# Performance work log

Measured on AMD Instinct MI355X. Metric: run time of the kernel, lower is better.

Reference implementation:

```python
import jax, jax.numpy as jnp
import numpy as np

HIDDEN = 2048
N_HEADS = 16
N_KV_HEADS = 4
HEAD_DIM = HIDDEN // N_HEADS  # 128
BATCH = 1
SEQ = 2048
EPS = 1e-6


def _rms_norm(x, scale, eps=EPS):
    var = jnp.mean(jnp.square(x), axis=-1, keepdims=True)
    return x * jax.lax.rsqrt(var + eps) * scale


def _rotate_half(x):
    x1, x2 = jnp.split(x, 2, axis=-1)
    return jnp.concatenate((-x2, x1), axis=-1)


def setup_inputs() -> dict:
    key = jax.random.key(0)
    ks = jax.random.split(key, 8)
    hidden_states = jax.random.normal(ks[0], (BATCH, SEQ, HIDDEN), dtype=jnp.float32)
    # causal mask, broadcastable over [B, H, S, S]
    attention_mask = jnp.tril(jnp.ones((SEQ, SEQ), dtype=bool))[None, None, :, :]
    # standard RoPE tables, broadcastable against [B, S, H, D]
    inv_freq = 1.0 / (10000.0 ** (np.arange(0, HEAD_DIM, 2, dtype=np.float32) / HEAD_DIM))
    t = np.arange(SEQ, dtype=np.float32)
    freqs = np.outer(t, inv_freq)                      # [S, D/2]
    emb = np.concatenate([freqs, freqs], axis=-1)      # [S, D]
    cos = jnp.asarray(np.cos(emb))[:, None, :]         # [S, 1, D]
    sin = jnp.asarray(np.sin(emb))[:, None, :]
    s = 1.0 / np.sqrt(HIDDEN)
    Wq = jax.random.normal(ks[1], (HIDDEN, N_HEADS * HEAD_DIM), dtype=jnp.float32) * s
    Wk = jax.random.normal(ks[2], (HIDDEN, N_KV_HEADS * HEAD_DIM), dtype=jnp.float32) * s
    Wv = jax.random.normal(ks[3], (HIDDEN, N_KV_HEADS * HEAD_DIM), dtype=jnp.float32) * s
    Wo = jax.random.normal(ks[4], (HIDDEN, HIDDEN), dtype=jnp.float32) * s
    q_norm_scale = jnp.ones((HEAD_DIM,), dtype=jnp.float32)
    k_norm_scale = jnp.ones((HEAD_DIM,), dtype=jnp.float32)
    last_norm_scale = jnp.ones((HIDDEN,), dtype=jnp.float32)
    return {
        "hidden_states": hidden_states,
        "cos": cos,
        "sin": sin,
        "Wq": Wq,
        "Wk": Wk,
        "Wv": Wv,
        "Wo": Wo,
        "q_norm_scale": q_norm_scale,
        "k_norm_scale": k_norm_scale,
        "last_norm_scale": last_norm_scale,
        "attention_mask": attention_mask,
    }


def reference(hidden_states, cos, sin, Wq, Wk, Wv, Wo,
              q_norm_scale, k_norm_scale, last_norm_scale, attention_mask):
    B, S, _ = hidden_states.shape
    q = (hidden_states @ Wq).reshape(B, S, N_HEADS, HEAD_DIM)
    k = (hidden_states @ Wk).reshape(B, S, N_KV_HEADS, HEAD_DIM)
    v = (hidden_states @ Wv).reshape(B, S, N_KV_HEADS, HEAD_DIM)
    # per-head RMSNorm on Q/K
    q = _rms_norm(q, q_norm_scale)
    k = _rms_norm(k, k_norm_scale)
    # RoPE (cos/sin broadcast [S,1,D] -> [B,S,H,D])
    q = q * cos + _rotate_half(q) * sin
    k = k * cos + _rotate_half(k) * sin
    # GQA expansion
    groups = N_HEADS // N_KV_HEADS
    if groups > 1:
        k = jnp.repeat(k, groups, axis=2)
        v = jnp.repeat(v, groups, axis=2)
    out = jax.nn.dot_product_attention(q, k, v, mask=attention_mask)  # [B,S,H,D]
    out = out.reshape(B, S, HIDDEN) @ Wo
    return _rms_norm(out, last_norm_scale)
```

## Files before the change

### kernel.cpp

```cpp
#include <hip/hip_runtime.h>

typedef unsigned short u16;
typedef unsigned int u32;

#define S 2048
#define HID 2048
#define NH 16
#define NKV 4
#define D 128
#define QKVP 3072
#define QSCALE (0.08838834764831845f * 1.4426950408889634f)
#define NEG_INF -3.0e38f

typedef __attribute__((ext_vector_type(8))) short short8;
typedef __attribute__((ext_vector_type(4))) float f32x4;

__device__ __forceinline__ float bf2f(u16 u) {
  union { u32 i; float f; } c; c.i = ((u32)u) << 16; return c.f;
}
__device__ __forceinline__ u16 f2bf(float f) {
  union { float f; u32 i; } c; c.f = f;
  u32 x = c.i;
  u32 r = x + 0x7fffu + ((x >> 16) & 1u);
  return (u16)(r >> 16);
}

#if __has_builtin(__builtin_amdgcn_exp2f)
__device__ __forceinline__ float exp2_hw(float x) { return __builtin_amdgcn_exp2f(x); }
#else
__device__ __forceinline__ float exp2_hw(float x) { return exp2f(x); }
#endif

__device__ __forceinline__ u32 cvt_pk_bf16(float a, float b) {
  u32 r;
  asm("v_cvt_pk_bf16_f32 %0, %1, %2" : "=v"(r) : "v"(a), "v"(b));
  return r;
}

__device__ __forceinline__ void gload16(const u16* g, u16* l) {
  __builtin_amdgcn_global_load_lds(
      (const __attribute__((address_space(1))) u32*)g,
      (__attribute__((address_space(3))) u32*)l, 16, 0, 0);
}

__global__ __launch_bounds__(256) void k_cvt(const float* __restrict__ src,
                                             u16* __restrict__ dst) {
  int i = (blockIdx.x * 256 + threadIdx.x) * 8;
  float4 v0 = *(const float4*)(src + i);
  float4 v1 = *(const float4*)(src + i + 4);
  ushort4 w0, w1;
  w0.x = f2bf(v0.x); w0.y = f2bf(v0.y); w0.z = f2bf(v0.z); w0.w = f2bf(v0.w);
  w1.x = f2bf(v1.x); w1.y = f2bf(v1.y); w1.z = f2bf(v1.z); w1.w = f2bf(v1.w);
  *(ushort4*)(dst + i) = w0;
  *(ushort4*)(dst + i + 4) = w1;
}

__device__ __forceinline__ void transpose_body(const float* __restrict__ src,
                                               u16* __restrict__ dst,
                                               int N, int K, int nt, int kt,
                                               int t) {
  __shared__ float T[64][65];
#pragma unroll
  for (int it = 0; it < 4; ++it) {
    int r = it * 16 + (t >> 4), c = (t & 15) * 4;
    float4 v = *(const float4*)(src + (size_t)(kt + r) * N + nt + c);
    T[r][c] = v.x; T[r][c + 1] = v.y; T[r][c + 2] = v.z; T[r][c + 3] = v.w;
  }
  __syncthreads();
#pragma unroll
  for (int it = 0; it < 2; ++it) {
    int n = it * 32 + (t >> 3), k8 = (t & 7) * 8;
    ushort4 w0, w1;
    w0.x = f2bf(T[k8 + 0][n]); w0.y = f2bf(T[k8 + 1][n]);
    w0.z = f2bf(T[k8 + 2][n]); w0.w = f2bf(T[k8 + 3][n]);
    w1.x = f2bf(T[k8 + 4][n]); w1.y = f2bf(T[k8 + 5][n]);
    w1.z = f2bf(T[k8 + 6][n]); w1.w = f2bf(T[k8 + 7][n]);
    *(ushort4*)(dst + (size_t)(nt + n) * K + kt + k8) = w0;
    *(ushort4*)(dst + (size_t)(nt + n) * K + kt + k8 + 4) = w1;
  }
}

__global__ __launch_bounds__(256) void k_transpose(const float* __restrict__ src,
                                                   u16* __restrict__ dst,
                                                   int N, int K) {
  transpose_body(src, dst, N, K, blockIdx.x * 64, blockIdx.y * 64, threadIdx.x);
}

__global__ __launch_bounds__(256) void k_transpose_qkv(const float* __restrict__ Wq,
                                                       const float* __restrict__ Wk,
                                                       const float* __restrict__ Wv,
                                                       u16* __restrict__ WT) {
  const int bx = blockIdx.x;
  const float* src; u16* dst; int N, nt;
  if (bx < 32)      { src = Wq; dst = WT;                    N = 2048; nt = bx * 64; }
  else if (bx < 40) { src = Wk; dst = WT + 2048ull * 2048;   N = 512;  nt = (bx - 32) * 64; }
  else              { src = Wv; dst = WT + 2560ull * 2048;   N = 512;  nt = (bx - 40) * 64; }
  transpose_body(src, dst, N, 2048, nt, blockIdx.y * 64, threadIdx.x);
}

__global__ __launch_bounds__(256) void k_vt(const u16* __restrict__ QKV,
                                            u16* __restrict__ Vt) {
  __shared__ u16 T[64][66];
  const int t = threadIdx.x;
  const int s0 = blockIdx.x * 64, d0 = blockIdx.y * 64;
#pragma unroll
  for (int it = 0; it < 4; ++it) {
    int r = it * 16 + (t >> 4), c = (t & 15) * 4;
    ushort4 v = *(const ushort4*)(QKV + (size_t)(s0 + r) * QKVP + 2560 + d0 + c);
    T[r][c] = v.x; T[r][c + 1] = v.y; T[r][c + 2] = v.z; T[r][c + 3] = v.w;
  }
  __syncthreads();
#pragma unroll
  for (int it = 0; it < 4; ++it) {
    int dd = it * 16 + (t >> 4), sc = (t & 15) * 4;
    ushort4 w;
    w.x = T[sc + 0][dd]; w.y = T[sc + 1][dd];
    w.z = T[sc + 2][dd]; w.w = T[sc + 3][dd];
    *(ushort4*)(Vt + (size_t)(d0 + dd) * S + s0 + sc) = w;
  }
}

__global__ __launch_bounds__(256) void k_gemm_mfma(const u16* __restrict__ A,
                                                   const u16* __restrict__ BT,
                                                   void* __restrict__ Cout,
                                                   int N, int K, int out_bf16) {
  __shared__ __align__(16) u16 As[2][128 * 32];
  __shared__ __align__(16) u16 Bs[2][128 * 32];
  const int t = threadIdx.x, w = t >> 6, lane = t & 63;
  const int l15 = lane & 15, quad = lane >> 4;
  const int m0 = blockIdx.y * 128, n0 = blockIdx.x * 128;
  const int wr = w >> 1, wc = w & 1;

  const int sr = w * 16 + (lane >> 2);
  const int sk8 = (lane & 3) * 8;
  const u16* Ag0 = A + (size_t)(m0 + sr) * K + sk8;
  const u16* Ag1 = A + (size_t)(m0 + 64 + sr) * K + sk8;
  const u16* Bg0 = BT + (size_t)(n0 + sr) * K + sk8;
  const u16* Bg1 = BT + (size_t)(n0 + 64 + sr) * K + sk8;

  f32x4 acc[4][4];
#pragma unroll
  for (int i = 0; i < 4; ++i)
#pragma unroll
    for (int j = 0; j < 4; ++j) acc[i][j] = (f32x4){0.f, 0.f, 0.f, 0.f};

  auto STAGE = [&](int k0, int b) {
    gload16(Ag0 + k0, &As[b][w * 512]);
    gload16(Ag1 + k0, &As[b][2048 + w * 512]);
    gload16(Bg0 + k0, &Bs[b][w * 512]);
    gload16(Bg1 + k0, &Bs[b][2048 + w * 512]);
  };

  STAGE(0, 0);
  __syncthreads();
  int cur = 0;
  for (int k0 = 0; k0 < K; k0 += 32) {
    if (k0 + 32 < K) STAGE(k0 + 32, cur ^ 1);

    short8 af[4], bf[4];
#pragma unroll
    for (int i = 0; i < 4; ++i)
      af[i] = *(const short8*)&As[cur][(wr * 64 + i * 16 + l15) * 32 + quad * 8];
#pragma unroll
    for (int j = 0; j < 4; ++j)
      bf[j] = *(const short8*)&Bs[cur][(wc * 64 + j * 16 + l15) * 32 + quad * 8];
#pragma unroll
    for (int i = 0; i < 4; ++i)
#pragma unroll
      for (int j = 0; j < 4; ++j)
        acc[i][j] = __builtin_amdgcn_mfma_f32_16x16x32_bf16(af[i], bf[j], acc[i][j], 0, 0, 0);

    __syncthreads();
    cur ^= 1;
  }

  if (out_bf16) {
    u16* C = (u16*)Cout;
#pragma unroll
    for (int i = 0; i < 4; ++i)
#pragma unroll
      for (int j = 0; j < 4; ++j) {
        int col = n0 + wc * 64 + j * 16 + l15;
#pragma unroll
        for (int r = 0; r < 4; ++r)
          C[(size_t)(m0 + wr * 64 + i * 16 + quad * 4 + r) * N + col] = f2bf(acc[i][j][r]);
      }
  } else {
    float* C = (float*)Cout;
#pragma unroll
    for (int i = 0; i < 4; ++i)
#pragma unroll
      for (int j = 0; j < 4; ++j) {
        int col = n0 + wc * 64 + j * 16 + l15;
#pragma unroll
        for (int r = 0; r < 4; ++r)
          C[(size_t)(m0 + wr * 64 + i * 16 + quad * 4 + r) * N + col] = acc[i][j][r];
      }
  }
}

__global__ __launch_bounds__(128) void k_norm_rope(u16* __restrict__ QKV,
                                                   const float* __restrict__ qsc,
                                                   const float* __restrict__ ksc,
                                                   const float* __restrict__ cosp,
                                                   const float* __restrict__ sinp) {
  const int s = blockIdx.x, hh = blockIdx.y, d = threadIdx.x;
  u16* row; const float* sc; float scale;
  if (hh < NH) { row = QKV + (size_t)s * QKVP + hh * D;            sc = qsc; scale = QSCALE; }
  else         { row = QKV + (size_t)s * QKVP + 2048 + (hh - NH) * D; sc = ksc; scale = 1.0f; }
  float x = bf2f(row[d]);
  float v = x * x;
#pragma unroll
  for (int o = 32; o; o >>= 1) v += __shfl_xor(v, o, 64);
  __shared__ float red[2];
  if ((d & 63) == 0) red[d >> 6] = v;
  __syncthreads();
  float var = (red[0] + red[1]) * (1.0f / 128.0f);
  float rinv = rsqrtf(var + 1e-6f) * scale;
  float xn = x * rinv * sc[d];
  __shared__ float sh[D];
  sh[d] = xn;
  __syncthreads();
  float rot = (d < 64) ? -sh[d + 64] : sh[d - 64];
  row[d] = f2bf(xn * cosp[s * D + d] + rot * sinp[s * D + d]);
}

#define KP 128
#define PTP 72

__global__ __launch_bounds__(256) void k_flash(const u16* __restrict__ QKV,
                                               const u16* __restrict__ Vt,
                                               u16* __restrict__ O) {
  const int h = blockIdx.y, g = h >> 2;
  const int qt = (h < 8) ? (31 - (int)blockIdx.x) : (int)blockIdx.x;
  const int t = threadIdx.x;
  const int w = t >> 6, lane = t & 63, l15 = lane & 15, quad = lane >> 4;

  __shared__ __align__(16) u16 Klds[2][64 * KP];
  __shared__ __align__(16) u16 Pt[4][16 * PTP];

  const int qbase = qt * 64 + w * 16;
  const int qrow = qbase + l15;

  short8 qf[4];
  {
    const u16* qp = QKV + (size_t)qrow * QKVP + h * D + quad * 8;
#pragma unroll
    for (int c = 0; c < 4; ++c) qf[c] = *(const short8*)(qp + c * 32);
  }

  float m = NEG_INF, l = 0.f;
  f32x4 oacc[8];
#pragma unroll
  for (int nc = 0; nc < 8; ++nc) oacc[nc] = (f32x4){0.f, 0.f, 0.f, 0.f};

  const int nt = qt + 1;

  auto KLOAD = [&](int j0, int b) {
#pragma unroll
    for (int it = 0; it < 4; ++it) {
      int rl = w * 16 + it * 4 + quad;
      int gchunk = (lane & 15) ^ (rl & 7);
      const u16* gp = QKV + (size_t)(j0 + rl) * QKVP + 2048 + g * D + gchunk * 8;
      gload16(gp, &Klds[b][(w * 16 + it * 4) * KP]);
    }
  };

  KLOAD(0, 0);
  for (int jt = 0; jt < nt; ++jt) {
    const int b = jt & 1;
    __syncthreads();
    if (jt + 1 < nt) KLOAD((jt + 1) * 64, b ^ 1);

    const int j0 = jt * 64;
    const u16* vbase = Vt + (size_t)g * D * S + j0;

    short8 vf0[8];
#pragma unroll
    for (int nc = 0; nc < 8; ++nc)
      vf0[nc] = *(const short8*)(vbase + (size_t)(nc * 16 + l15) * S + quad * 8);

    f32x4 sa[4];
#pragma unroll
    for (int sub = 0; sub < 4; ++sub) {
      f32x4 acc = {0.f, 0.f, 0.f, 0.f};
#pragma unroll
      for (int c = 0; c < 4; ++c) {
        int ch = (c * 4 + quad) ^ (l15 & 7);
        short8 kf = *(const short8*)&Klds[b][(sub * 16 + l15) * KP + ch * 8];
        acc = __builtin_amdgcn_mfma_f32_16x16x32_bf16(kf, qf[c], acc, 0, 0, 0);
      }
      sa[sub] = acc;
    }

    short8 vf1[8];
#pragma unroll
    for (int nc = 0; nc < 8; ++nc)
      vf1[nc] = *(const short8*)(vbase + (size_t)(nc * 16 + l15) * S + 32 + quad * 8);

    if (jt == nt - 1) {
#pragma unroll
      for (int sub = 0; sub < 4; ++sub) {
        int keyb = j0 + sub * 16 + quad * 4;
#pragma unroll
        for (int r = 0; r < 4; ++r)
          if (keyb + r > qrow) sa[sub][r] = NEG_INF;
      }
    }

    float tmax = sa[0][0];
#pragma unroll
    for (int sub = 0; sub < 4; ++sub)
#pragma unroll
      for (int r = 0; r < 4; ++r) tmax = fmaxf(tmax, sa[sub][r]);
    tmax = fmaxf(tmax, __shfl_xor(tmax, 16, 64));
    tmax = fmaxf(tmax, __shfl_xor(tmax, 32, 64));
    if (jt == 0 || !__all(tmax - m <= 8.f)) {
      float mn = (jt == 0) ? tmax : fmaxf(m, tmax);
      float alpha = (jt == 0) ? 0.f : exp2_hw(m - mn);
      m = mn;
      l *= alpha;
#pragma unroll
      for (int nc = 0; nc < 8; ++nc) {
        oacc[nc][0] *= alpha; oacc[nc][1] *= alpha;
        oacc[nc][2] *= alpha; oacc[nc][3] *= alpha;
      }
    }
    float rs = 0.f;
#pragma unroll
    for (int sub = 0; sub < 4; ++sub) {
      float p0 = exp2_hw(sa[sub][0] - m);
      float p1 = exp2_hw(sa[sub][1] - m);
      float p2 = exp2_hw(sa[sub][2] - m);
      float p3 = exp2_hw(sa[sub][3] - m);
      rs += (p0 + p1) + (p2 + p3);
      u32 lo = cvt_pk_bf16(p0, p1);
      u32 hi = cvt_pk_bf16(p2, p3);
      *(uint2*)&Pt[w][l15 * PTP + sub * 16 + quad * 4] = make_uint2(lo, hi);
    }
    rs += __shfl_xor(rs, 16, 64);
    rs += __shfl_xor(rs, 32, 64);
    l += rs;

    {
      short8 pf0 = *(const short8*)&Pt[w][l15 * PTP + quad * 8];
      short8 pf1 = *(const short8*)&Pt[w][l15 * PTP + 32 + quad * 8];
#pragma unroll
      for (int nc = 0; nc < 8; ++nc)
        oacc[nc] = __builtin_amdgcn_mfma_f32_16x16x32_bf16(vf0[nc], pf0, oacc[nc], 0, 0, 0);
#pragma unroll
      for (int nc = 0; nc < 8; ++nc)
        oacc[nc] = __builtin_amdgcn_mfma_f32_16x16x32_bf16(vf1[nc], pf1, oacc[nc], 0, 0, 0);
    }
  }

  float inv = 1.0f / l;
  u16* orow = O + (size_t)qrow * HID + h * D;
#pragma unroll
  for (int nc = 0; nc < 8; ++nc) {
    ushort4 wv;
    wv.x = f2bf(oacc[nc][0] * inv); wv.y = f2bf(oacc[nc][1] * inv);
    wv.z = f2bf(oacc[nc][2] * inv); wv.w = f2bf(oacc[nc][3] * inv);
    *(ushort4*)(orow + nc * 16 + quad * 4) = wv;
  }
}

__device__ __forceinline__ float blockSum256(float v, float* red, int t) {
#pragma unroll
  for (int o = 32; o; o >>= 1) v += __shfl_xor(v, o, 64);
  if ((t & 63) == 0) red[t >> 6] = v;
  __syncthreads();
  v = red[0] + red[1] + red[2] + red[3];
  __syncthreads();
  return v;
}

__global__ __launch_bounds__(256) void k_fnorm(const float* __restrict__ X,
                                               const float* __restrict__ sc,
                                               float* __restrict__ out) {
  const int s = blockIdx.x, t = threadIdx.x;
  const float* row = X + (size_t)s * HID;
  float4 r0 = *(const float4*)(row + t * 8);
  float4 r1 = *(const float4*)(row + t * 8 + 4);
  float x[8] = {r0.x, r0.y, r0.z, r0.w, r1.x, r1.y, r1.z, r1.w};
  float ss = 0.f;
#pragma unroll
  for (int ii = 0; ii < 8; ++ii) ss += x[ii] * x[ii];
  __shared__ float red[4];
  float tot = blockSum256(ss, red, t);
  float rinv = rsqrtf(tot * (1.0f / 2048.0f) + 1e-6f);
  float4 s0 = *(const float4*)(sc + t * 8);
  float4 s1 = *(const float4*)(sc + t * 8 + 4);
  float4 w0 = make_float4(x[0] * rinv * s0.x, x[1] * rinv * s0.y,
                          x[2] * rinv * s0.z, x[3] * rinv * s0.w);
  float4 w1 = make_float4(x[4] * rinv * s1.x, x[5] * rinv * s1.y,
                          x[6] * rinv * s1.z, x[7] * rinv * s1.w);
  *(float4*)(out + (size_t)s * HID + t * 8) = w0;
  *(float4*)(out + (size_t)s * HID + t * 8 + 4) = w1;
}

extern "C" void kernel_launch(void* const* d_in, const int* in_sizes, int n_in,
                              void* d_out, int out_size, void* d_ws, size_t ws_size,
                              hipStream_t stream) {
  const float* hidden = (const float*)d_in[0];
  const float* cosp   = (const float*)d_in[1];
  const float* sinp   = (const float*)d_in[2];
  const float* Wq     = (const float*)d_in[3];
  const float* Wk     = (const float*)d_in[4];
  const float* Wv     = (const float*)d_in[5];
  const float* Wo     = (const float*)d_in[6];
  const float* qsc    = (const float*)d_in[7];
  const float* ksc    = (const float*)d_in[8];
  const float* lsc    = (const float*)d_in[9];
  float* out = (float*)d_out;

  char* ws = (char*)d_ws;
  u16*   Hb  = (u16*)(ws);
  u16*   WoT = (u16*)(ws);
  u16*   WT  = (u16*)(ws + (8ull << 20));
  u16*   An  = (u16*)(ws + (8ull << 20));
  u16*   QKV = (u16*)(ws + (20ull << 20));
  float* Ob  = (float*)(ws + (20ull << 20));
  u16*   Vtb = (u16*)(ws + (32ull << 20));

  k_cvt<<<S * HID / (256 * 8), 256, 0, stream>>>(hidden, Hb);
  k_transpose_qkv<<<dim3(48, 32), 256, 0, stream>>>(Wq, Wk, Wv, WT);
  k_gemm_mfma<<<dim3(24, 16), 256, 0, stream>>>(Hb, WT, QKV, QKVP, 2048, 1);
  k_transpose<<<dim3(32, 32), 256, 0, stream>>>(Wo, WoT, 2048, 2048);
  k_norm_rope<<<dim3(S, NH + NKV), 128, 0, stream>>>(QKV, qsc, ksc, cosp, sinp);
  k_vt<<<dim3(32, 8), 256, 0, stream>>>(QKV, Vtb);
  k_flash<<<dim3(32, NH), 256, 0, stream>>>(QKV, Vtb, An);
  k_gemm_mfma<<<dim3(16, 16), 256, 0, stream>>>(An, WoT, Ob, 2048, 2048, 0);
  k_fnorm<<<S, 256, 0, stream>>>(Ob, lsc, out);
}
```

Measured before the change: 333.0 us.

## Widen GEMM K-tile with swizzled LDS and use per-wave K tiles in flash attention

The GEMM K step doubles from 32 to 64 with an XOR-swizzled LDS layout, so there are half as many barriers per K and fewer LDS bank conflicts. Flash attention now gives each wave its own 32-key K buffer, double-buffered and synchronised with vmcnt waits instead of block barriers. Each wave also stops at its own causal limit rather than the block's, which skips masked work. The trade-offs are more LDS per block, duplicated K loads across waves, and smaller MFMA batches per iteration.

```diff
diff --git a/kernel.cpp b/kernel.cpp
--- a/kernel.cpp
+++ b/kernel.cpp
@@ -124,19 +124,17 @@
                                                    const u16* __restrict__ BT,
                                                    void* __restrict__ Cout,
                                                    int N, int K, int out_bf16) {
-  __shared__ __align__(16) u16 As[2][128 * 32];
-  __shared__ __align__(16) u16 Bs[2][128 * 32];
+  __shared__ __align__(16) u16 As[2][128 * 64];
+  __shared__ __align__(16) u16 Bs[2][128 * 64];
   const int t = threadIdx.x, w = t >> 6, lane = t & 63;
   const int l15 = lane & 15, quad = lane >> 4;
   const int m0 = blockIdx.y * 128, n0 = blockIdx.x * 128;
   const int wr = w >> 1, wc = w & 1;
 
-  const int sr = w * 16 + (lane >> 2);
-  const int sk8 = (lane & 3) * 8;
-  const u16* Ag0 = A + (size_t)(m0 + sr) * K + sk8;
-  const u16* Ag1 = A + (size_t)(m0 + 64 + sr) * K + sk8;
-  const u16* Bg0 = BT + (size_t)(n0 + sr) * K + sk8;
-  const u16* Bg1 = BT + (size_t)(n0 + 64 + sr) * K + sk8;
+  const int srow = lane >> 3;
+  const int schunk = (lane & 7) ^ srow;
+  const u16* Agb = A + (size_t)(m0 + w * 8 + srow) * K + schunk * 8;
+  const u16* Bgb = BT + (size_t)(n0 + w * 8 + srow) * K + schunk * 8;
 
   f32x4 acc[4][4];
 #pragma unroll
@@ -145,30 +143,35 @@
     for (int j = 0; j < 4; ++j) acc[i][j] = (f32x4){0.f, 0.f, 0.f, 0.f};
 
   auto STAGE = [&](int k0, int b) {
-    gload16(Ag0 + k0, &As[b][w * 512]);
-    gload16(Ag1 + k0, &As[b][2048 + w * 512]);
-    gload16(Bg0 + k0, &Bs[b][w * 512]);
-    gload16(Bg1 + k0, &Bs[b][2048 + w * 512]);
+#pragma unroll
+    for (int it = 0; it < 4; ++it) {
+      gload16(Agb + (size_t)it * 32 * K + k0, &As[b][(w * 8 + it * 32) * 64]);
+      gload16(Bgb + (size_t)it * 32 * K + k0, &Bs[b][(w * 8 + it * 32) * 64]);
+    }
   };
 
   STAGE(0, 0);
   __syncthreads();
   int cur = 0;
-  for (int k0 = 0; k0 < K; k0 += 32) {
-    if (k0 + 32 < K) STAGE(k0 + 32, cur ^ 1);
-
-    short8 af[4], bf[4];
+  for (int k0 = 0; k0 < K; k0 += 64) {
+    if (k0 + 64 < K) STAGE(k0 + 64, cur ^ 1);
+
+    short8 af[4][2], bf[4][2];
 #pragma unroll
     for (int i = 0; i < 4; ++i)
-      af[i] = *(const short8*)&As[cur][(wr * 64 + i * 16 + l15) * 32 + quad * 8];
-#pragma unroll
-    for (int j = 0; j < 4; ++j)
-      bf[j] = *(const short8*)&Bs[cur][(wc * 64 + j * 16 + l15) * 32 + quad * 8];
-#pragma unroll
-    for (int i = 0; i < 4; ++i)
-#pragma unroll
-      for (int j = 0; j < 4; ++j)
-        acc[i][j] = __builtin_amdgcn_mfma_f32_16x16x32_bf16(af[i], bf[j], acc[i][j], 0, 0, 0);
+#pragma unroll
+      for (int k2 = 0; k2 < 2; ++k2) {
+        int ch = (k2 * 4 + quad) ^ (l15 & 7);
+        af[i][k2] = *(const short8*)&As[cur][(wr * 64 + i * 16 + l15) * 64 + ch * 8];
+        bf[i][k2] = *(const short8*)&Bs[cur][(wc * 64 + i * 16 + l15) * 64 + ch * 8];
+      }
+#pragma unroll
+    for (int k2 = 0; k2 < 2; ++k2)
+#pragma unroll
+      for (int i = 0; i < 4; ++i)
+#pragma unroll
+        for (int j = 0; j < 4; ++j)
+          acc[i][j] = __builtin_amdgcn_mfma_f32_16x16x32_bf16(af[i][k2], bf[j][k2], acc[i][j], 0, 0, 0);
 
     __syncthreads();
     cur ^= 1;
@@ -225,6 +228,7 @@
   row[d] = f2bf(xn * cosp[s * D + d] + rot * sinp[s * D + d]);
 }
 
+#define KVB 32
 #define KP 128
 #define PTP 72
 
@@ -236,11 +240,12 @@
   const int t = threadIdx.x;
   const int w = t >> 6, lane = t & 63, l15 = lane & 15, quad = lane >> 4;
 
-  __shared__ __align__(16) u16 Klds[2][64 * KP];
+  __shared__ __align__(16) u16 Klds[4][2][KVB * KP];
   __shared__ __align__(16) u16 Pt[4][16 * PTP];
 
-  const int qbase = qt * 64 + w * 16;
-  const int qrow = qbase + l15;
+  u16* Kw[2] = {&Klds[w][0][0], &Klds[w][1][0]};
+
+  const int qrow = qt * 64 + w * 16 + l15;
 
   short8 qf[4];
   {
@@ -254,53 +259,52 @@
 #pragma unroll
   for (int nc = 0; nc < 8; ++nc) oacc[nc] = (f32x4){0.f, 0.f, 0.f, 0.f};
 
-  const int nt = qt + 1;
-
-  auto KLOAD = [&](int j0, int b) {
-#pragma unroll
-    for (int it = 0; it < 4; ++it) {
-      int rl = w * 16 + it * 4 + quad;
-      int gchunk = (lane & 15) ^ (rl & 7);
+  const int nt = ((qt * 64 + w * 16 + 15) >> 5) + 1;
+
+  auto KLOAD = [&](int j0, u16* dst) {
+#pragma unroll
+    for (int it = 0; it < 8; ++it) {
+      int rl = it * 4 + quad;
+      int gchunk = l15 ^ (rl & 7);
       const u16* gp = QKV + (size_t)(j0 + rl) * QKVP + 2048 + g * D + gchunk * 8;
-      gload16(gp, &Klds[b][(w * 16 + it * 4) * KP]);
+      gload16(gp, dst + (it * 4) * KP);
     }
   };
 
-  KLOAD(0, 0);
+  KLOAD(0, Kw[0]);
   for (int jt = 0; jt < nt; ++jt) {
-    const int b = jt & 1;
-    __syncthreads();
-    if (jt + 1 < nt) KLOAD((jt + 1) * 64, b ^ 1);
-
-    const int j0 = jt * 64;
+    const u16* kb = Kw[jt & 1];
+    if (jt + 1 < nt) {
+      KLOAD((jt + 1) * KVB, Kw[(jt & 1) ^ 1]);
+      asm volatile("s_waitcnt vmcnt(8)" ::: "memory");
+    } else {
+      asm volatile("s_waitcnt vmcnt(0)" ::: "memory");
+    }
+
+    const int j0 = jt * KVB;
     const u16* vbase = Vt + (size_t)g * D * S + j0;
 
-    short8 vf0[8];
+    short8 vf[8];
 #pragma unroll
     for (int nc = 0; nc < 8; ++nc)
-      vf0[nc] = *(const short8*)(vbase + (size_t)(nc * 16 + l15) * S + quad * 8);
-
-    f32x4 sa[4];
-#pragma unroll
-    for (int sub = 0; sub < 4; ++sub) {
+      vf[nc] = *(const short8*)(vbase + (size_t)(nc * 16 + l15) * S + quad * 8);
+
+    f32x4 sa[2];
+#pragma unroll
+    for (int sub = 0; sub < 2; ++sub) {
       f32x4 acc = {0.f, 0.f, 0.f, 0.f};
 #pragma unroll
       for (int c = 0; c < 4; ++c) {
         int ch = (c * 4 + quad) ^ (l15 & 7);
-        short8 kf = *(const short8*)&Klds[b][(sub * 16 + l15) * KP + ch * 8];
+        short8 kf = *(const short8*)&kb[(sub * 16 + l15) * KP + ch * 8];
         acc = __builtin_amdgcn_mfma_f32_16x16x32_bf16(kf, qf[c], acc, 0, 0, 0);
       }
       sa[sub] = acc;
     }
 
-    short8 vf1[8];
-#pragma unroll
-    for (int nc = 0; nc < 8; ++nc)
-      vf1[nc] = *(const short8*)(vbase + (size_t)(nc * 16 + l15) * S + 32 + quad * 8);
-
     if (jt == nt - 1) {
 #pragma unroll
-      for (int sub = 0; sub < 4; ++sub) {
+      for (int sub = 0; sub < 2; ++sub) {
         int keyb = j0 + sub * 16 + quad * 4;
 #pragma unroll
         for (int r = 0; r < 4; ++r)
@@ -310,7 +314,7 @@
 
     float tmax = sa[0][0];
 #pragma unroll
-    for (int sub = 0; sub < 4; ++sub)
+    for (int sub = 0; sub < 2; ++sub)
 #pragma unroll
       for (int r = 0; r < 4; ++r) tmax = fmaxf(tmax, sa[sub][r]);
     tmax = fmaxf(tmax, __shfl_xor(tmax, 16, 64));
@@ -328,7 +332,7 @@
     }
     float rs = 0.f;
 #pragma unroll
-    for (int sub = 0; sub < 4; ++sub) {
+    for (int sub = 0; sub < 2; ++sub) {
       float p0 = exp2_hw(sa[sub][0] - m);
       float p1 = exp2_hw(sa[sub][1] - m);
       float p2 = exp2_hw(sa[sub][2] - m);
@@ -343,14 +347,10 @@
     l += rs;
 
     {
-      short8 pf0 = *(const short8*)&Pt[w][l15 * PTP + quad * 8];
-      short8 pf1 = *(const short8*)&Pt[w][l15 * PTP + 32 + quad * 8];
+      short8 pf = *(const short8*)&Pt[w][l15 * PTP + quad * 8];
 #pragma unroll
       for (int nc = 0; nc < 8; ++nc)
-        oacc[nc] = __builtin_amdgcn_mfma_f32_16x16x32_bf16(vf0[nc], pf0, oacc[nc], 0, 0, 0);
-#pragma unroll
-      for (int nc = 0; nc < 8; ++nc)
-        oacc[nc] = __builtin_amdgcn_mfma_f32_16x16x32_bf16(vf1[nc], pf1, oacc[nc], 0, 0, 0);
+        oacc[nc] = __builtin_amdgcn_mfma_f32_16x16x32_bf16(vf[nc], pf, oacc[nc], 0, 0, 0);
     }
   }
 
```

After: 307.5 us. 7.7% less time.
